# Kernel optimization log

Measured on AMD Instinct MI355X. Metric: run time of the kernel, lower is better.

Reference implementation:

```python
import jax, jax.numpy as jnp
import numpy as np

N_NODES = 100000
N_EDGES = 1600000
IN_DIM, HID, OUT = 6, 64, 32


def _linear_params(key, fan_in, fan_out):
    k1, k2 = jax.random.split(key)
    bound = 1.0 / np.sqrt(fan_in)
    W = jax.random.uniform(k1, (fan_in, fan_out), jnp.float32, -bound, bound)
    b = jax.random.uniform(k2, (fan_out,), jnp.float32, -bound, bound)
    return W, b


def setup_inputs() -> dict:
    key = jax.random.key(0)
    ks = jax.random.split(key, 9)
    x = jax.random.normal(ks[0], (N_NODES, IN_DIM), jnp.float32)
    edge_index = jax.random.randint(ks[1], (2, N_EDGES), 0, N_NODES, jnp.int64)
    edge_attr = jax.random.normal(ks[2], (N_EDGES, 3), jnp.float32)
    W1a, b1a = _linear_params(ks[3], IN_DIM + 3, HID)
    W1b, b1b = _linear_params(ks[4], HID, HID)
    W2a, b2a = _linear_params(ks[5], HID + 3, HID)
    W2b, b2b = _linear_params(ks[6], HID, HID)
    W3a, b3a = _linear_params(ks[7], HID + 3, OUT)
    W3b, b3b = _linear_params(ks[8], OUT, OUT)
    return {
        "x": x, "edge_index": edge_index, "edge_attr": edge_attr,
        "W1a": W1a, "b1a": b1a, "W1b": W1b, "b1b": b1b,
        "W2a": W2a, "b2a": b2a, "W2b": W2b, "b2b": b2b,
        "W3a": W3a, "b3a": b3a, "W3b": W3b, "b3b": b3b,
    }


def _gnn_layer(x, src, dst, edge_attr, Wa, ba, Wb, bb):
    # message: per-edge 2-layer MLP on [x_j, edge_attr]
    msg = jnp.concatenate([x[src], edge_attr], axis=-1)       # [E, in+3]
    h = jax.nn.relu(msg @ Wa + ba) @ Wb + bb                   # [E, out]
    # aggr='mean': scatter-sum into target nodes, divide by in-degree
    s = jax.ops.segment_sum(h, dst, num_segments=N_NODES)     # [N, out]
    cnt = jax.ops.segment_sum(jnp.ones((src.shape[0],), x.dtype), dst,
                              num_segments=N_NODES)
    return s / jnp.maximum(cnt, 1.0)[:, None]


def reference(x, edge_index, edge_attr,
              W1a, b1a, W1b, b1b,
              W2a, b2a, W2b, b2b,
              W3a, b3a, W3b, b3b):
    src, dst = edge_index[0], edge_index[1]   # x_j = x[src], aggregate at dst
    h = _gnn_layer(x, src, dst, edge_attr, W1a, b1a, W1b, b1b)
    h = jax.nn.relu(h)
    h = _gnn_layer(h, src, dst, edge_attr, W2a, b2a, W2b, b2b)
    h = jax.nn.relu(h)
    out = _gnn_layer(h, src, dst, edge_attr, W3a, b3a, W3b, b3b)
    return out
```

## Files before the change

kernel.cpp:

```cpp
#include <hip/hip_runtime.h>
#include <hip/hip_fp16.h>

#define N_NODES 100000
#define N_EDGES 1600000

__global__ __launch_bounds__(256) void degree_kernel(const int* __restrict__ dst,
                                                     int* __restrict__ cnt, int E) {
    const int range = blockIdx.x & 7;
    const int lo = range * (N_NODES / 8);
    const int hi = lo + (N_NODES / 8);
    int i = (blockIdx.x >> 3) * blockDim.x + threadIdx.x;
    const int stride = (gridDim.x >> 3) * blockDim.x;
    for (; i < E; i += stride) {
        const int d = dst[i];
        if (d >= lo && d < hi) atomicAdd(&cnt[d], 1);
    }
}

__global__ __launch_bounds__(256) void inv_kernel(const int* __restrict__ cnt,
                                                  float* __restrict__ inv, int N) {
    int i = blockIdx.x * blockDim.x + threadIdx.x;
    if (i < N) inv[i] = (cnt[i] > 0) ? (1.0f / (float)cnt[i]) : 0.0f;
}

__global__ __launch_bounds__(256) void block_sum_kernel(const int* __restrict__ cnt,
                                                        int* __restrict__ bsum, int N) {
    __shared__ int s[256];
    const int tid = threadIdx.x;
    const int i = blockIdx.x * 256 + tid;
    s[tid] = (i < N) ? cnt[i] : 0;
    __syncthreads();
#pragma unroll
    for (int d = 128; d > 0; d >>= 1) {
        if (tid < d) s[tid] += s[tid + d];
        __syncthreads();
    }
    if (tid == 0) bsum[blockIdx.x] = s[0];
}

__global__ __launch_bounds__(512) void scan_bsum_kernel(int* __restrict__ bsum, int NB) {
    __shared__ int s[512];
    const int tid = threadIdx.x;
    const int v = (tid < NB) ? bsum[tid] : 0;
    s[tid] = v;
    __syncthreads();
    for (int d = 1; d < 512; d <<= 1) {
        const int t = (tid >= d) ? s[tid - d] : 0;
        __syncthreads();
        s[tid] += t;
        __syncthreads();
    }
    if (tid < NB) bsum[tid] = s[tid] - v;
}

__global__ __launch_bounds__(256) void make_cursor_kernel(const int* __restrict__ cnt,
                                                          const int* __restrict__ bsum,
                                                          int* __restrict__ cursor, int N) {
    __shared__ int s[256];
    const int tid = threadIdx.x;
    const int i = blockIdx.x * 256 + tid;
    const int v = (i < N) ? cnt[i] : 0;
    s[tid] = v;
    __syncthreads();
    for (int d = 1; d < 256; d <<= 1) {
        const int t = (tid >= d) ? s[tid - d] : 0;
        __syncthreads();
        s[tid] += t;
        __syncthreads();
    }
    if (i < N) cursor[i] = bsum[blockIdx.x] + s[tid] - v;
}

__global__ __launch_bounds__(256) void scatter_pack_kernel(
    const int* __restrict__ src, const int* __restrict__ dst,
    const float* __restrict__ ea,
    int* __restrict__ cursor, float4* __restrict__ spf, int E) {
    const int range = blockIdx.x & 7;
    const int lo = range * (N_NODES / 8);
    const int hi = lo + (N_NODES / 8);
    int i = (blockIdx.x >> 3) * blockDim.x + threadIdx.x;
    const int stride = (gridDim.x >> 3) * blockDim.x;
    for (; i < E; i += stride) {
        const int d = dst[i];
        if (d >= lo && d < hi) {
            const int pos = atomicAdd(&cursor[d], 1);
            spf[pos] = make_float4(__int_as_float(src[i]),
                                   ea[3 * (size_t)i + 0],
                                   ea[3 * (size_t)i + 1],
                                   ea[3 * (size_t)i + 2]);
        }
    }
}

__global__ __launch_bounds__(256) void node_gemm6h(
    const float* __restrict__ x, const float* __restrict__ W,
    const float* __restrict__ bias, __half* __restrict__ out_, int N) {
    int n = blockIdx.x * blockDim.x + threadIdx.x;
    if (n >= N) return;
    const float* row = x + (size_t)n * 6;
    float v[6];
#pragma unroll
    for (int k = 0; k < 6; ++k) v[k] = row[k];
    __half2* orow = (__half2*)(out_ + (size_t)n * 64);
    for (int g = 0; g < 16; ++g) {
        float a0 = bias[4 * g + 0], a1 = bias[4 * g + 1];
        float a2 = bias[4 * g + 2], a3 = bias[4 * g + 3];
#pragma unroll
        for (int k = 0; k < 6; ++k) {
            const float m = v[k];
            const float* w = &W[k * 64 + 4 * g];
            a0 = fmaf(m, w[0], a0);
            a1 = fmaf(m, w[1], a1);
            a2 = fmaf(m, w[2], a2);
            a3 = fmaf(m, w[3], a3);
        }
        orow[2 * g]     = __floats2half2_rn(a0, a1);
        orow[2 * g + 1] = __floats2half2_rn(a2, a3);
    }
}

template <int DNEXT, bool OUTH>
__global__ __launch_bounds__(256) void fused_agg64(
    const __half* __restrict__ P,
    const float4* __restrict__ spf,
    const int* __restrict__ cursor, const int* __restrict__ cnt,
    const float* __restrict__ inv,
    const float* __restrict__ We,
    const float* __restrict__ Wb,
    const float* __restrict__ bb,
    const float* __restrict__ Wn,
    const float* __restrict__ bn,
    void* __restrict__ Poutv, int N) {
    const int lane = threadIdx.x & 63;
    const int w    = threadIdx.x >> 6;
    const int sub  = lane >> 3;
    const int p    = lane & 7;
    const int n    = blockIdx.x * 4 + w;

    __shared__ __align__(16) float lrow[4][64];

    float we0[8], we1[8], we2[8];
#pragma unroll
    for (int k = 0; k < 8; ++k) {
        we0[k] = We[0 * 64 + 8 * p + k];
        we1[k] = We[1 * 64 + 8 * p + k];
        we2[k] = We[2 * 64 + 8 * p + k];
    }

    const int end   = cursor[n];
    const int count = cnt[n];
    int j = end - count;
    const float s_inv = inv[n];
    const float mask  = (s_inv != 0.0f) ? 1.0f : 0.0f;

    float s0 = 0.f, s1 = 0.f, s2 = 0.f, s3 = 0.f;
    float s4 = 0.f, s5 = 0.f, s6 = 0.f, s7 = 0.f;

#define GRP8(base, valid)                                                        \
    {                                                                            \
        const int ei = (base) + sub;                                             \
        const float4 f = spf[ei < end ? ei : end - 1];                           \
        const float4 rawf = *(const float4*)((const __half*)P +                  \
                            ((size_t)__float_as_int(f.x) << 6) + 8 * p);         \
        const __half2* hp = (const __half2*)&rawf;                               \
        const float2 q0 = __half22float2(hp[0]);                                 \
        const float2 q1 = __half22float2(hp[1]);                                 \
        const float2 q2 = __half22float2(hp[2]);                                 \
        const float2 q3 = __half22float2(hp[3]);                                 \
        const float h0 = fmaxf(fmaf(f.w, we2[0], fmaf(f.z, we1[0], fmaf(f.y, we0[0], q0.x))), 0.f); \
        const float h1 = fmaxf(fmaf(f.w, we2[1], fmaf(f.z, we1[1], fmaf(f.y, we0[1], q0.y))), 0.f); \
        const float h2 = fmaxf(fmaf(f.w, we2[2], fmaf(f.z, we1[2], fmaf(f.y, we0[2], q1.x))), 0.f); \
        const float h3 = fmaxf(fmaf(f.w, we2[3], fmaf(f.z, we1[3], fmaf(f.y, we0[3], q1.y))), 0.f); \
        const float h4 = fmaxf(fmaf(f.w, we2[4], fmaf(f.z, we1[4], fmaf(f.y, we0[4], q2.x))), 0.f); \
        const float h5 = fmaxf(fmaf(f.w, we2[5], fmaf(f.z, we1[5], fmaf(f.y, we0[5], q2.y))), 0.f); \
        const float h6 = fmaxf(fmaf(f.w, we2[6], fmaf(f.z, we1[6], fmaf(f.y, we0[6], q3.x))), 0.f); \
        const float h7 = fmaxf(fmaf(f.w, we2[7], fmaf(f.z, we1[7], fmaf(f.y, we0[7], q3.y))), 0.f); \
        if (valid) {                                                             \
            s0 += h0; s1 += h1; s2 += h2; s3 += h3;                              \
            s4 += h4; s5 += h5; s6 += h6; s7 += h7;                              \
        }                                                                        \
    }

    for (; j + 16 <= end; j += 16) { GRP8(j, true) GRP8(j + 8, true) }
    if (j + 8 <= end) { GRP8(j, true) j += 8; }
    {
        const int rem = end - j;
        if (rem > 0) { GRP8(j, (sub < rem)) }
    }
#undef GRP8

#define RED(d) \
    s0 += __shfl_xor(s0, d); s1 += __shfl_xor(s1, d); \
    s2 += __shfl_xor(s2, d); s3 += __shfl_xor(s3, d); \
    s4 += __shfl_xor(s4, d); s5 += __shfl_xor(s5, d); \
    s6 += __shfl_xor(s6, d); s7 += __shfl_xor(s7, d);
    RED(8) RED(16) RED(32)
#undef RED

    if (lane < 8) {
        *(float4*)&lrow[w][8 * p] =
            make_float4(s0 * s_inv, s1 * s_inv, s2 * s_inv, s3 * s_inv);
        *(float4*)&lrow[w][8 * p + 4] =
            make_float4(s4 * s_inv, s5 * s_inv, s6 * s_inv, s7 * s_inv);
    }
    __builtin_amdgcn_wave_barrier();

    float m = bb[lane] * mask;
#pragma unroll
    for (int k = 0; k < 16; ++k) {
        const float4 r = *(const float4*)&lrow[w][4 * k];
        m = fmaf(r.x, Wb[(4 * k + 0) * 64 + lane], m);
        m = fmaf(r.y, Wb[(4 * k + 1) * 64 + lane], m);
        m = fmaf(r.z, Wb[(4 * k + 2) * 64 + lane], m);
        m = fmaf(r.w, Wb[(4 * k + 3) * 64 + lane], m);
    }
    m = fmaxf(m, 0.0f);
    __builtin_amdgcn_wave_barrier();
    lrow[w][lane] = m;
    __builtin_amdgcn_wave_barrier();
    const int c2 = lane % DNEXT;
    float o = bn[c2];
#pragma unroll
    for (int k = 0; k < 16; ++k) {
        const float4 r = *(const float4*)&lrow[w][4 * k];
        o = fmaf(r.x, Wn[(4 * k + 0) * DNEXT + c2], o);
        o = fmaf(r.y, Wn[(4 * k + 1) * DNEXT + c2], o);
        o = fmaf(r.z, Wn[(4 * k + 2) * DNEXT + c2], o);
        o = fmaf(r.w, Wn[(4 * k + 3) * DNEXT + c2], o);
    }
    if (lane < DNEXT) {
        if constexpr (OUTH)
            ((__half*)Poutv)[(size_t)n * DNEXT + lane] = __float2half_rn(o);
        else
            ((float*)Poutv)[(size_t)n * DNEXT + lane] = o;
    }
}

__global__ __launch_bounds__(256) void fused_agg32h(
    const __half* __restrict__ P,
    const float4* __restrict__ spf,
    const int* __restrict__ cursor, const int* __restrict__ cnt,
    const float* __restrict__ inv,
    const float* __restrict__ We,
    const float* __restrict__ Wb,
    const float* __restrict__ bb,
    float* __restrict__ out, int N) {
    const int lane = threadIdx.x & 63;
    const int w    = threadIdx.x >> 6;
    const int sub  = lane >> 2;
    const int p    = lane & 3;
    const int n    = blockIdx.x * 4 + w;

    __shared__ __align__(16) float lrow[4][32];

    float we0[8], we1[8], we2[8];
#pragma unroll
    for (int k = 0; k < 8; ++k) {
        we0[k] = We[0 * 32 + 8 * p + k];
        we1[k] = We[1 * 32 + 8 * p + k];
        we2[k] = We[2 * 32 + 8 * p + k];
    }

    const int end   = cursor[n];
    const int count = cnt[n];
    int j = end - count;
    const float s_inv = inv[n];
    const float mask  = (s_inv != 0.0f) ? 1.0f : 0.0f;

    float s0 = 0.f, s1 = 0.f, s2 = 0.f, s3 = 0.f;
    float s4 = 0.f, s5 = 0.f, s6 = 0.f, s7 = 0.f;

#define GRP16(base, valid)                                                       \
    {                                                                            \
        const int ei = (base) + sub;                                             \
        const float4 f = spf[ei < end ? ei : end - 1];                           \
        const float4 rawf = *(const float4*)((const __half*)P +                  \
                            ((size_t)__float_as_int(f.x) << 5) + 8 * p);         \
        const __half2* hp = (const __half2*)&rawf;                               \
        const float2 q0 = __half22float2(hp[0]);                                 \
        const float2 q1 = __half22float2(hp[1]);                                 \
        const float2 q2 = __half22float2(hp[2]);                                 \
        const float2 q3 = __half22float2(hp[3]);                                 \
        const float h0 = fmaxf(fmaf(f.w, we2[0], fmaf(f.z, we1[0], fmaf(f.y, we0[0], q0.x))), 0.f); \
        const float h1 = fmaxf(fmaf(f.w, we2[1], fmaf(f.z, we1[1], fmaf(f.y, we0[1], q0.y))), 0.f); \
        const float h2 = fmaxf(fmaf(f.w, we2[2], fmaf(f.z, we1[2], fmaf(f.y, we0[2], q1.x))), 0.f); \
        const float h3 = fmaxf(fmaf(f.w, we2[3], fmaf(f.z, we1[3], fmaf(f.y, we0[3], q1.y))), 0.f); \
        const float h4 = fmaxf(fmaf(f.w, we2[4], fmaf(f.z, we1[4], fmaf(f.y, we0[4], q2.x))), 0.f); \
        const float h5 = fmaxf(fmaf(f.w, we2[5], fmaf(f.z, we1[5], fmaf(f.y, we0[5], q2.y))), 0.f); \
        const float h6 = fmaxf(fmaf(f.w, we2[6], fmaf(f.z, we1[6], fmaf(f.y, we0[6], q3.x))), 0.f); \
        const float h7 = fmaxf(fmaf(f.w, we2[7], fmaf(f.z, we1[7], fmaf(f.y, we0[7], q3.y))), 0.f); \
        if (valid) {                                                             \
            s0 += h0; s1 += h1; s2 += h2; s3 += h3;                              \
            s4 += h4; s5 += h5; s6 += h6; s7 += h7;                              \
        }                                                                        \
    }

    for (; j + 16 <= end; j += 16) { GRP16(j, true) }
    {
        const int rem = end - j;
        if (rem > 0) { GRP16(j, (sub < rem)) }
    }
#undef GRP16

#define RED(d) \
    s0 += __shfl_xor(s0, d); s1 += __shfl_xor(s1, d); \
    s2 += __shfl_xor(s2, d); s3 += __shfl_xor(s3, d); \
    s4 += __shfl_xor(s4, d); s5 += __shfl_xor(s5, d); \
    s6 += __shfl_xor(s6, d); s7 += __shfl_xor(s7, d);
    RED(4) RED(8) RED(16) RED(32)
#undef RED

    if (lane < 4) {
        *(float4*)&lrow[w][8 * p] =
            make_float4(s0 * s_inv, s1 * s_inv, s2 * s_inv, s3 * s_inv);
        *(float4*)&lrow[w][8 * p + 4] =
            make_float4(s4 * s_inv, s5 * s_inv, s6 * s_inv, s7 * s_inv);
    }
    __builtin_amdgcn_wave_barrier();

    const int c = lane & 31;
    float m = bb[c] * mask;
#pragma unroll
    for (int k = 0; k < 8; ++k) {
        const float4 r = *(const float4*)&lrow[w][4 * k];
        m = fmaf(r.x, Wb[(4 * k + 0) * 32 + c], m);
        m = fmaf(r.y, Wb[(4 * k + 1) * 32 + c], m);
        m = fmaf(r.z, Wb[(4 * k + 2) * 32 + c], m);
        m = fmaf(r.w, Wb[(4 * k + 3) * 32 + c], m);
    }
    if (lane < 32) out[(size_t)n * 32 + c] = m;
}

extern "C" void kernel_launch(void* const* d_in, const int* in_sizes, int n_in,
                              void* d_out, int out_size, void* d_ws, size_t ws_size,
                              hipStream_t stream) {
    const float* x   = (const float*)d_in[0];
    const int*   ei  = (const int*)d_in[1];
    const float* ea  = (const float*)d_in[2];
    const float* W1a = (const float*)d_in[3];
    const float* b1a = (const float*)d_in[4];
    const float* W1b = (const float*)d_in[5];
    const float* b1b = (const float*)d_in[6];
    const float* W2a = (const float*)d_in[7];
    const float* b2a = (const float*)d_in[8];
    const float* W2b = (const float*)d_in[9];
    const float* b2b = (const float*)d_in[10];
    const float* W3a = (const float*)d_in[11];
    const float* b3a = (const float*)d_in[12];
    const float* W3b = (const float*)d_in[13];
    const float* b3b = (const float*)d_in[14];

    const int* src = ei;
    const int* dst = ei + N_EDGES;
    float* out = (float*)d_out;

    char* ws = (char*)d_ws;
    int*    cnt    = (int*)(ws);
    float*  inv    = (float*)(ws + 0x80000);
    int*    bsum   = (int*)(ws + 0x100000);
    int*    cursor = (int*)(ws + 0x110000);
    float4* spf    = (float4*)(ws + 0x200000);
    __half* PH1    = (__half*)(ws + 0x1B00000);
    __half* PH2    = (__half*)(ws + 0x2800000);
    __half* P3h    = (__half*)(ws + 0x3500000);

    const int NBLK = (N_NODES + 255) / 256;

    hipMemsetAsync(cnt, 0, N_NODES * sizeof(int), stream);
    degree_kernel<<<2048, 256, 0, stream>>>(dst, cnt, N_EDGES);
    inv_kernel<<<NBLK, 256, 0, stream>>>(cnt, inv, N_NODES);
    block_sum_kernel<<<NBLK, 256, 0, stream>>>(cnt, bsum, N_NODES);
    scan_bsum_kernel<<<1, 512, 0, stream>>>(bsum, NBLK);
    make_cursor_kernel<<<NBLK, 256, 0, stream>>>(cnt, bsum, cursor, N_NODES);
    scatter_pack_kernel<<<2048, 256, 0, stream>>>(src, dst, ea, cursor, spf, N_EDGES);

    node_gemm6h<<<NBLK, 256, 0, stream>>>(x, W1a, b1a, PH1, N_NODES);

    fused_agg64<64, true><<<N_NODES / 4, 256, 0, stream>>>(
        PH1, spf, cursor, cnt, inv, W1a + 6 * 64, W1b, b1b, W2a, b2a, PH2, N_NODES);
    fused_agg64<32, true><<<N_NODES / 4, 256, 0, stream>>>(
        PH2, spf, cursor, cnt, inv, W2a + 64 * 64, W2b, b2b, W3a, b3a, P3h, N_NODES);
    fused_agg32h<<<N_NODES / 4, 256, 0, stream>>>(
        P3h, spf, cursor, cnt, inv, W3a + 64 * 32, W3b, b3b, out, N_NODES);
}
```

Baseline: 473.7 us.

## Split fused aggregate+MLP kernels into persistent aggregation and per-node MLP kernels

Removes the per-node dense MLP epilogue from the gather/aggregation kernels. Aggregation now runs as grid-stride persistent waves that write fp16 mean rows, and the Wb and next-layer Wa products move into separate thread-per-node MLP kernels. The aim is to keep the gather kernels lean and spread the dense work over a full-occupancy thread-per-node layout. The cost is extra kernel launches and extra fp16 intermediate round-trips through global memory, plus extra fp16 rounding of intermediates.

```diff
diff --git a/kernel.cpp b/kernel.cpp
--- a/kernel.cpp
+++ b/kernel.cpp
@@ -119,25 +119,18 @@
     }
 }
 
-template <int DNEXT, bool OUTH>
-__global__ __launch_bounds__(256) void fused_agg64(
+__global__ __launch_bounds__(256) void agg64_pure(
     const __half* __restrict__ P,
     const float4* __restrict__ spf,
     const int* __restrict__ cursor, const int* __restrict__ cnt,
     const float* __restrict__ inv,
     const float* __restrict__ We,
-    const float* __restrict__ Wb,
-    const float* __restrict__ bb,
-    const float* __restrict__ Wn,
-    const float* __restrict__ bn,
-    void* __restrict__ Poutv, int N) {
-    const int lane = threadIdx.x & 63;
-    const int w    = threadIdx.x >> 6;
-    const int sub  = lane >> 3;
-    const int p    = lane & 7;
-    const int n    = blockIdx.x * 4 + w;
-
-    __shared__ __align__(16) float lrow[4][64];
+    __half* __restrict__ A, int N) {
+    const int lane  = threadIdx.x & 63;
+    const int sub   = lane >> 3;
+    const int p     = lane & 7;
+    const int gw    = (blockIdx.x * blockDim.x + threadIdx.x) >> 6;
+    const int nwave = (gridDim.x * blockDim.x) >> 6;
 
     float we0[8], we1[8], we2[8];
 #pragma unroll
@@ -147,14 +140,14 @@
         we2[k] = We[2 * 64 + 8 * p + k];
     }
 
-    const int end   = cursor[n];
-    const int count = cnt[n];
-    int j = end - count;
-    const float s_inv = inv[n];
-    const float mask  = (s_inv != 0.0f) ? 1.0f : 0.0f;
-
-    float s0 = 0.f, s1 = 0.f, s2 = 0.f, s3 = 0.f;
-    float s4 = 0.f, s5 = 0.f, s6 = 0.f, s7 = 0.f;
+    for (int n = gw; n < N; n += nwave) {
+        const int end   = cursor[n];
+        const int count = cnt[n];
+        int j = end - count;
+        const float s_inv = inv[n];
+
+        float s0 = 0.f, s1 = 0.f, s2 = 0.f, s3 = 0.f;
+        float s4 = 0.f, s5 = 0.f, s6 = 0.f, s7 = 0.f;
 
 #define GRP8(base, valid)                                                        \
     {                                                                            \
@@ -181,77 +174,46 @@
         }                                                                        \
     }
 
-    for (; j + 16 <= end; j += 16) { GRP8(j, true) GRP8(j + 8, true) }
-    if (j + 8 <= end) { GRP8(j, true) j += 8; }
-    {
-        const int rem = end - j;
-        if (rem > 0) { GRP8(j, (sub < rem)) }
-    }
+        for (; j + 16 <= end; j += 16) { GRP8(j, true) GRP8(j + 8, true) }
+        if (j + 8 <= end) { GRP8(j, true) j += 8; }
+        {
+            const int rem = end - j;
+            if (rem > 0) { GRP8(j, (sub < rem)) }
+        }
 #undef GRP8
 
 #define RED(d) \
-    s0 += __shfl_xor(s0, d); s1 += __shfl_xor(s1, d); \
-    s2 += __shfl_xor(s2, d); s3 += __shfl_xor(s3, d); \
-    s4 += __shfl_xor(s4, d); s5 += __shfl_xor(s5, d); \
-    s6 += __shfl_xor(s6, d); s7 += __shfl_xor(s7, d);
-    RED(8) RED(16) RED(32)
+        s0 += __shfl_xor(s0, d); s1 += __shfl_xor(s1, d); \
+        s2 += __shfl_xor(s2, d); s3 += __shfl_xor(s3, d); \
+        s4 += __shfl_xor(s4, d); s5 += __shfl_xor(s5, d); \
+        s6 += __shfl_xor(s6, d); s7 += __shfl_xor(s7, d);
+        RED(8) RED(16) RED(32)
 #undef RED
 
-    if (lane < 8) {
-        *(float4*)&lrow[w][8 * p] =
-            make_float4(s0 * s_inv, s1 * s_inv, s2 * s_inv, s3 * s_inv);
-        *(float4*)&lrow[w][8 * p + 4] =
-            make_float4(s4 * s_inv, s5 * s_inv, s6 * s_inv, s7 * s_inv);
-    }
-    __builtin_amdgcn_wave_barrier();
-
-    float m = bb[lane] * mask;
-#pragma unroll
-    for (int k = 0; k < 16; ++k) {
-        const float4 r = *(const float4*)&lrow[w][4 * k];
-        m = fmaf(r.x, Wb[(4 * k + 0) * 64 + lane], m);
-        m = fmaf(r.y, Wb[(4 * k + 1) * 64 + lane], m);
-        m = fmaf(r.z, Wb[(4 * k + 2) * 64 + lane], m);
-        m = fmaf(r.w, Wb[(4 * k + 3) * 64 + lane], m);
-    }
-    m = fmaxf(m, 0.0f);
-    __builtin_amdgcn_wave_barrier();
-    lrow[w][lane] = m;
-    __builtin_amdgcn_wave_barrier();
-    const int c2 = lane % DNEXT;
-    float o = bn[c2];
-#pragma unroll
-    for (int k = 0; k < 16; ++k) {
-        const float4 r = *(const float4*)&lrow[w][4 * k];
-        o = fmaf(r.x, Wn[(4 * k + 0) * DNEXT + c2], o);
-        o = fmaf(r.y, Wn[(4 * k + 1) * DNEXT + c2], o);
-        o = fmaf(r.z, Wn[(4 * k + 2) * DNEXT + c2], o);
-        o = fmaf(r.w, Wn[(4 * k + 3) * DNEXT + c2], o);
-    }
-    if (lane < DNEXT) {
-        if constexpr (OUTH)
-            ((__half*)Poutv)[(size_t)n * DNEXT + lane] = __float2half_rn(o);
-        else
-            ((float*)Poutv)[(size_t)n * DNEXT + lane] = o;
-    }
-}
-
-__global__ __launch_bounds__(256) void fused_agg32h(
+        if (lane < 8) {
+            __half2 h01 = __floats2half2_rn(s0 * s_inv, s1 * s_inv);
+            __half2 h23 = __floats2half2_rn(s2 * s_inv, s3 * s_inv);
+            __half2 h45 = __floats2half2_rn(s4 * s_inv, s5 * s_inv);
+            __half2 h67 = __floats2half2_rn(s6 * s_inv, s7 * s_inv);
+            union { __half2 h[4]; float4 f; } u;
+            u.h[0] = h01; u.h[1] = h23; u.h[2] = h45; u.h[3] = h67;
+            *(float4*)(A + (size_t)n * 64 + 8 * p) = u.f;
+        }
+    }
+}
+
+__global__ __launch_bounds__(256) void agg32_pure(
     const __half* __restrict__ P,
     const float4* __restrict__ spf,
     const int* __restrict__ cursor, const int* __restrict__ cnt,
     const float* __restrict__ inv,
     const float* __restrict__ We,
-    const float* __restrict__ Wb,
-    const float* __restrict__ bb,
-    float* __restrict__ out, int N) {
-    const int lane = threadIdx.x & 63;
-    const int w    = threadIdx.x >> 6;
-    const int sub  = lane >> 2;
-    const int p    = lane & 3;
-    const int n    = blockIdx.x * 4 + w;
-
-    __shared__ __align__(16) float lrow[4][32];
+    __half* __restrict__ A, int N) {
+    const int lane  = threadIdx.x & 63;
+    const int sub   = lane >> 2;
+    const int p     = lane & 3;
+    const int gw    = (blockIdx.x * blockDim.x + threadIdx.x) >> 6;
+    const int nwave = (gridDim.x * blockDim.x) >> 6;
 
     float we0[8], we1[8], we2[8];
 #pragma unroll
@@ -261,14 +223,14 @@
         we2[k] = We[2 * 32 + 8 * p + k];
     }
 
-    const int end   = cursor[n];
-    const int count = cnt[n];
-    int j = end - count;
-    const float s_inv = inv[n];
-    const float mask  = (s_inv != 0.0f) ? 1.0f : 0.0f;
-
-    float s0 = 0.f, s1 = 0.f, s2 = 0.f, s3 = 0.f;
-    float s4 = 0.f, s5 = 0.f, s6 = 0.f, s7 = 0.f;
+    for (int n = gw; n < N; n += nwave) {
+        const int end   = cursor[n];
+        const int count = cnt[n];
+        int j = end - count;
+        const float s_inv = inv[n];
+
+        float s0 = 0.f, s1 = 0.f, s2 = 0.f, s3 = 0.f;
+        float s4 = 0.f, s5 = 0.f, s6 = 0.f, s7 = 0.f;
 
 #define GRP16(base, valid)                                                       \
     {                                                                            \
@@ -295,40 +257,116 @@
         }                                                                        \
     }
 
-    for (; j + 16 <= end; j += 16) { GRP16(j, true) }
-    {
-        const int rem = end - j;
-        if (rem > 0) { GRP16(j, (sub < rem)) }
-    }
+        for (; j + 16 <= end; j += 16) { GRP16(j, true) }
+        {
+            const int rem = end - j;
+            if (rem > 0) { GRP16(j, (sub < rem)) }
+        }
 #undef GRP16
 
 #define RED(d) \
-    s0 += __shfl_xor(s0, d); s1 += __shfl_xor(s1, d); \
-    s2 += __shfl_xor(s2, d); s3 += __shfl_xor(s3, d); \
-    s4 += __shfl_xor(s4, d); s5 += __shfl_xor(s5, d); \
-    s6 += __shfl_xor(s6, d); s7 += __shfl_xor(s7, d);
-    RED(4) RED(8) RED(16) RED(32)
+        s0 += __shfl_xor(s0, d); s1 += __shfl_xor(s1, d); \
+        s2 += __shfl_xor(s2, d); s3 += __shfl_xor(s3, d); \
+        s4 += __shfl_xor(s4, d); s5 += __shfl_xor(s5, d); \
+        s6 += __shfl_xor(s6, d); s7 += __shfl_xor(s7, d);
+        RED(4) RED(8) RED(16) RED(32)
 #undef RED
 
-    if (lane < 4) {
-        *(float4*)&lrow[w][8 * p] =
-            make_float4(s0 * s_inv, s1 * s_inv, s2 * s_inv, s3 * s_inv);
-        *(float4*)&lrow[w][8 * p + 4] =
-            make_float4(s4 * s_inv, s5 * s_inv, s6 * s_inv, s7 * s_inv);
-    }
-    __builtin_amdgcn_wave_barrier();
-
-    const int c = lane & 31;
-    float m = bb[c] * mask;
-#pragma unroll
-    for (int k = 0; k < 8; ++k) {
-        const float4 r = *(const float4*)&lrow[w][4 * k];
-        m = fmaf(r.x, Wb[(4 * k + 0) * 32 + c], m);
-        m = fmaf(r.y, Wb[(4 * k + 1) * 32 + c], m);
-        m = fmaf(r.z, Wb[(4 * k + 2) * 32 + c], m);
-        m = fmaf(r.w, Wb[(4 * k + 3) * 32 + c], m);
-    }
-    if (lane < 32) out[(size_t)n * 32 + c] = m;
+        if (lane < 4) {
+            __half2 h01 = __floats2half2_rn(s0 * s_inv, s1 * s_inv);
+            __half2 h23 = __floats2half2_rn(s2 * s_inv, s3 * s_inv);
+            __half2 h45 = __floats2half2_rn(s4 * s_inv, s5 * s_inv);
+            __half2 h67 = __floats2half2_rn(s6 * s_inv, s7 * s_inv);
+            union { __half2 h[4]; float4 f; } u;
+            u.h[0] = h01; u.h[1] = h23; u.h[2] = h45; u.h[3] = h67;
+            *(float4*)(A + (size_t)n * 32 + 8 * p) = u.f;
+        }
+    }
+}
+
+template <int IN, int OUT, bool RELU, bool MASK>
+__global__ __launch_bounds__(256) void node_mlp_h(
+    const __half* __restrict__ in_, const float* __restrict__ W,
+    const float* __restrict__ bias, const float* __restrict__ inv,
+    __half* __restrict__ out_, int N) {
+    int n = blockIdx.x * blockDim.x + threadIdx.x;
+    if (n >= N) return;
+    const __half* row = in_ + (size_t)n * IN;
+    float v[IN];
+#pragma unroll
+    for (int q = 0; q < IN / 8; ++q) {
+        float4 raw = ((const float4*)row)[q];
+        const __half2* hp = (const __half2*)&raw;
+#pragma unroll
+        for (int t = 0; t < 4; ++t) {
+            const float2 f2 = __half22float2(hp[t]);
+            v[8 * q + 2 * t]     = f2.x;
+            v[8 * q + 2 * t + 1] = f2.y;
+        }
+    }
+    float bs = 1.0f;
+    if constexpr (MASK) bs = (inv[n] != 0.0f) ? 1.0f : 0.0f;
+
+    __half2 hout[OUT / 2];
+    for (int g = 0; g < OUT / 4; ++g) {
+        float a0 = bias[4 * g + 0] * bs, a1 = bias[4 * g + 1] * bs;
+        float a2 = bias[4 * g + 2] * bs, a3 = bias[4 * g + 3] * bs;
+#pragma unroll
+        for (int k = 0; k < IN; ++k) {
+            const float m = v[k];
+            const float* w = &W[k * OUT + 4 * g];
+            a0 = fmaf(m, w[0], a0);
+            a1 = fmaf(m, w[1], a1);
+            a2 = fmaf(m, w[2], a2);
+            a3 = fmaf(m, w[3], a3);
+        }
+        if (RELU) {
+            a0 = fmaxf(a0, 0.f); a1 = fmaxf(a1, 0.f);
+            a2 = fmaxf(a2, 0.f); a3 = fmaxf(a3, 0.f);
+        }
+        hout[2 * g]     = __floats2half2_rn(a0, a1);
+        hout[2 * g + 1] = __floats2half2_rn(a2, a3);
+    }
+    float4* orow = (float4*)(out_ + (size_t)n * OUT);
+#pragma unroll
+    for (int q = 0; q < OUT / 8; ++q) orow[q] = ((const float4*)hout)[q];
+}
+
+__global__ __launch_bounds__(256) void node_mlp_final(
+    const __half* __restrict__ in_, const float* __restrict__ W,
+    const float* __restrict__ bias, const float* __restrict__ inv,
+    float* __restrict__ out_, int N) {
+    int n = blockIdx.x * blockDim.x + threadIdx.x;
+    if (n >= N) return;
+    const __half* row = in_ + (size_t)n * 32;
+    float v[32];
+#pragma unroll
+    for (int q = 0; q < 4; ++q) {
+        float4 raw = ((const float4*)row)[q];
+        const __half2* hp = (const __half2*)&raw;
+#pragma unroll
+        for (int t = 0; t < 4; ++t) {
+            const float2 f2 = __half22float2(hp[t]);
+            v[8 * q + 2 * t]     = f2.x;
+            v[8 * q + 2 * t + 1] = f2.y;
+        }
+    }
+    const float bs = (inv[n] != 0.0f) ? 1.0f : 0.0f;
+    float* orow = out_ + (size_t)n * 32;
+    for (int g = 0; g < 8; ++g) {
+        float a0 = bias[4 * g + 0] * bs, a1 = bias[4 * g + 1] * bs;
+        float a2 = bias[4 * g + 2] * bs, a3 = bias[4 * g + 3] * bs;
+#pragma unroll
+        for (int k = 0; k < 32; ++k) {
+            const float m = v[k];
+            const float* w = &W[k * 32 + 4 * g];
+            a0 = fmaf(m, w[0], a0);
+            a1 = fmaf(m, w[1], a1);
+            a2 = fmaf(m, w[2], a2);
+            a3 = fmaf(m, w[3], a3);
+        }
+        ((float4*)orow)[g] = make_float4(a0, a1, a2, a3);
+    }
 }
 
 extern "C" void kernel_launch(void* const* d_in, const int* in_sizes, int n_in,
@@ -360,11 +398,12 @@
     int*    bsum   = (int*)(ws + 0x100000);
     int*    cursor = (int*)(ws + 0x110000);
     float4* spf    = (float4*)(ws + 0x200000);
-    __half* PH1    = (__half*)(ws + 0x1B00000);
-    __half* PH2    = (__half*)(ws + 0x2800000);
-    __half* P3h    = (__half*)(ws + 0x3500000);
+    __half* b0     = (__half*)(ws + 0x1B00000);
+    __half* b1     = (__half*)(ws + 0x2800000);
+    __half* b2     = (__half*)(ws + 0x3500000);
 
     const int NBLK = (N_NODES + 255) / 256;
+    const int ABLK = 1024;
 
     hipMemsetAsync(cnt, 0, N_NODES * sizeof(int), stream);
     degree_kernel<<<2048, 256, 0, stream>>>(dst, cnt, N_EDGES);
@@ -374,12 +413,16 @@
     make_cursor_kernel<<<NBLK, 256, 0, stream>>>(cnt, bsum, cursor, N_NODES);
     scatter_pack_kernel<<<2048, 256, 0, stream>>>(src, dst, ea, cursor, spf, N_EDGES);
 
-    node_gemm6h<<<NBLK, 256, 0, stream>>>(x, W1a, b1a, PH1, N_NODES);
-
-    fused_agg64<64, true><<<N_NODES / 4, 256, 0, stream>>>(
-        PH1, spf, cursor, cnt, inv, W1a + 6 * 64, W1b, b1b, W2a, b2a, PH2, N_NODES);
-    fused_agg64<32, true><<<N_NODES / 4, 256, 0, stream>>>(
-        PH2, spf, cursor, cnt, inv, W2a + 64 * 64, W2b, b2b, W3a, b3a, P3h, N_NODES);
-    fused_agg32h<<<N_NODES / 4, 256, 0, stream>>>(
-        P3h, spf, cursor, cnt, inv, W3a + 64 * 32, W3b, b3b, out, N_NODES);
-}
+    node_gemm6h<<<NBLK, 256, 0, stream>>>(x, W1a, b1a, b0, N_NODES);
+
+    agg64_pure<<<ABLK, 256, 0, stream>>>(b0, spf, cursor, cnt, inv, W1a + 6 * 64, b1, N_NODES);
+    node_mlp_h<64, 64, true, true><<<NBLK, 256, 0, stream>>>(b1, W1b, b1b, inv, b2, N_NODES);
+    node_mlp_h<64, 64, false, false><<<NBLK, 256, 0, stream>>>(b2, W2a, b2a, inv, b0, N_NODES);
+
+    agg64_pure<<<ABLK, 256, 0, stream>>>(b0, spf, cursor, cnt, inv, W2a + 64 * 64, b1, N_NODES);
+    node_mlp_h<64, 64, true, true><<<NBLK, 256, 0, stream>>>(b1, W2b, b2b, inv, b2, N_NODES);
+    node_mlp_h<64, 32, false, false><<<NBLK, 256, 0, stream>>>(b2, W3a, b3a, inv, b0, N_NODES);
+
+    agg32_pure<<<ABLK, 256, 0, stream>>>(b0, spf, cursor, cnt, inv, W3a + 64 * 32, b1, N_NODES);
+    node_mlp_final<<<NBLK, 256, 0, stream>>>(b1, W3b, b3b, inv, out, N_NODES);
+}
```

Measured after the change: 467.5 us. Within noise of the previous version (-1.3%).
